# Optimization experiments

Hardware: AMD Instinct MI355X
Metric: run time of the kernel (lower is better)

The kernel has to match this reference:

```python
import jax, jax.numpy as jnp
import numpy as np

B, S, H, D = 1, 2048, 16, 64
IN = 1024
STATE = H * D          # 1024
OUT = 1024
N_LAYERS = 24
EPS = 1e-6


def _rms(t):
    # RMSNorm without affine over last dim
    return t * jax.lax.rsqrt(jnp.mean(t * t, axis=-1, keepdims=True) + EPS)


def setup_inputs() -> dict:
    key = jax.random.key(0)
    ks = jax.random.split(key, 6)
    std = 0.02
    return {
        "x": jax.random.normal(ks[0], (B, S, IN), jnp.float32),
        # input_projection.weight^T: [in, 5*state]  (q|k|v|f|gate)
        "W_in": jax.random.normal(ks[1], (IN, 5 * STATE), jnp.float32) * std,
        "state_weight": jax.random.normal(ks[2], (H, D, D), jnp.float32) * std,
        "forget_multiplier": jax.random.normal(ks[3], (H, D), jnp.float32) * std,
        "logistic_factor": jnp.zeros((H,), jnp.float32),
        "g_norm_weight": jnp.ones((STATE,), jnp.float32),
        "W_out": jax.random.normal(ks[4], (STATE, OUT), jnp.float32) * (std / np.sqrt(2 * N_LAYERS)),
    }


def reference(x, W_in, state_weight, forget_multiplier, logistic_factor, g_norm_weight, W_out):
    proj = x @ W_in                                        # [B,S,5*STATE]
    q, k, v, f, gate = jnp.split(proj, [STATE, 2 * STATE, 3 * STATE, 4 * STATE], axis=-1)
    q = _rms(q.reshape(B, S, H, D))
    k = _rms(k.reshape(B, S, H, D))
    v = _rms(v.reshape(B, S, H, D))
    f = f.reshape(B, S, H, D)

    factor = jax.nn.sigmoid(logistic_factor)               # [H]
    # kvT[b,s,h,i,j] = k_i * (v_j * factor_h)
    kv = k[..., :, None] * (v * factor[None, None, :, None])[..., None, :]   # [B,S,H,D,D]
    # forget gate input, row-wise (depends on k-index i only)
    fg = jax.nn.sigmoid(f * (2.0 * jax.nn.sigmoid(forget_multiplier)))       # [B,S,H,D]
    rg = jax.nn.sigmoid(jnp.asarray(20.0, x.dtype))        # reset_input hardcoded to 20 -> ~1
    W = state_weight * factor[:, None, None]               # [H,D,D]

    def step(state, inp):
        kv_t, f_t = inp                                    # [B,H,D,D], [B,H,D]
        state = f_t[..., None] * jnp.einsum('bhik,hkj->bhij', state, W) + rg * kv_t
        return state, state

    xs = (kv.transpose(1, 0, 2, 3, 4), fg.transpose(1, 0, 2, 3))
    state0 = jnp.zeros((B, H, D, D), x.dtype)
    _, states = jax.lax.scan(step, state0, xs)             # [S,B,H,D,D]

    o = jnp.einsum('bshi,sbhij->bshj', q, states).reshape(B, S, STATE)
    y = o * jax.nn.silu(gate)
    y = _rms(y) * g_norm_weight                            # g_norm (affine RMSNorm)
    return y @ W_out
```

## Files before the change

kernel.cpp:

```cpp
#include <hip/hip_runtime.h>
#include <hip/hip_bf16.h>
#include <cstdint>


typedef __attribute__((ext_vector_type(8))) short short8;
typedef __attribute__((ext_vector_type(4))) short short4v;
typedef __attribute__((ext_vector_type(4))) float f32x4;

#define S_  2048
#define H_  16
#define NPROJ_ 5120

__device__ __forceinline__ float bf2f(unsigned short u) {
  unsigned int x = ((unsigned int)u) << 16;
  return __builtin_bit_cast(float, x);
}
__device__ __forceinline__ unsigned short f2bf(float f) {
  unsigned int x = __builtin_bit_cast(unsigned int, f);
  unsigned int r = (x + 0x7fffu + ((x >> 16) & 1u)) >> 16;
  return (unsigned short)r;
}
__device__ __forceinline__ float sigm(float x) { return 1.f / (1.f + __expf(-x)); }

__device__ __forceinline__ void gload_lds16(unsigned short* lds, const unsigned short* g) {
  __builtin_amdgcn_global_load_lds(
      (const __attribute__((address_space(1))) unsigned int*)g,
      (__attribute__((address_space(3))) unsigned int*)lds, 16, 0, 0);
}

__global__ __launch_bounds__(256) void k_prep(const float* __restrict__ x,
                                              const float* __restrict__ Win,
                                              const float* __restrict__ Wout,
                                              const float* __restrict__ sw,
                                              const float* __restrict__ lf,
                                              unsigned short* __restrict__ xbf,
                                              unsigned short* __restrict__ WinT,
                                              unsigned short* __restrict__ WoutT,
                                              unsigned short* __restrict__ Wt) {
  const int b = blockIdx.x, tid = threadIdx.x;
  if (b < 1536) {
    __shared__ float tile[64][65];
    const float* src; unsigned short* dst; int C, idx;
    if (b < 1280) { src = Win; dst = WinT; C = 5120; idx = b; }
    else          { src = Wout; dst = WoutT; C = 1024; idx = b - 1280; }
    const int R = 1024;
    int nct = C >> 6;
    int bc = idx % nct, br = idx / nct;
    int r0 = br * 64, c0 = bc * 64;
    int col = tid & 63, q = tid >> 6;
#pragma unroll
    for (int i = 0; i < 16; ++i) {
      int row = q * 16 + i;
      tile[row][col] = src[(size_t)(r0 + row) * C + c0 + col];
    }
    __syncthreads();
#pragma unroll
    for (int i = 0; i < 16; ++i) {
      int crow = q * 16 + i;
      dst[(size_t)(c0 + crow) * R + r0 + col] = f2bf(tile[col][crow]);
    }
  } else if (b < 2560) {
    int i = ((b - 1536) * 256 + tid) * 8;
    float4 v0 = *reinterpret_cast<const float4*>(x + i);
    float4 v1 = *reinterpret_cast<const float4*>(x + i + 4);
    uint4 o;
    o.x = (unsigned)f2bf(v0.x) | ((unsigned)f2bf(v0.y) << 16);
    o.y = (unsigned)f2bf(v0.z) | ((unsigned)f2bf(v0.w) << 16);
    o.z = (unsigned)f2bf(v1.x) | ((unsigned)f2bf(v1.y) << 16);
    o.w = (unsigned)f2bf(v1.z) | ((unsigned)f2bf(v1.w) << 16);
    *reinterpret_cast<uint4*>(xbf + i) = o;
  } else {
    int h = b - 2560;
    float factor = sigm(lf[h]);
    int j = tid >> 2, kq = (tid & 3) << 4;
#pragma unroll 4
    for (int k = kq; k < kq + 16; ++k)
      Wt[((size_t)h * 64 + j) * 64 + k] = f2bf(sw[((size_t)h * 64 + k) * 64 + j] * factor);
  }
}

__global__ __launch_bounds__(256) void k_gemm1_fused(
    const unsigned short* __restrict__ A, const unsigned short* __restrict__ BT,
    const float* __restrict__ fm, const float* __restrict__ lf,
    unsigned short* __restrict__ qnb, unsigned short* __restrict__ knb,
    unsigned short* __restrict__ vtb, unsigned short* __restrict__ fgb,
    unsigned short* __restrict__ sgb) {
  __shared__ __attribute__((aligned(16))) unsigned short As[3][128 * 32];
  __shared__ __attribute__((aligned(16))) unsigned short Bs[3][128 * 32];
  const int K = 1024;
  const int tid = threadIdx.x, w = tid >> 6, l = tid & 63;
  const int bx = blockIdx.x;
  const int m0 = (bx / 40) * 128, n0 = (bx % 40) * 128;
  const int wrow = (w >> 1) * 64, wcol = (w & 1) * 64;
  const int l15 = l & 15, lq = l >> 4;
  const int swzoff = l15 * 32 + ((lq ^ ((l15 >> 1) & 3)) * 8);
  f32x4 acc[4][4] = {};
  const int c0 = w * 2;
  const int srow0 = c0 * 16 + (l >> 2);
  const int scol = ((l & 3) ^ ((l >> 3) & 3)) * 8;
  const unsigned short* ga0 = A + (size_t)(m0 + srow0) * K + scol;
  const unsigned short* ga1 = ga0 + 16 * K;
  const unsigned short* gb0 = BT + (size_t)(n0 + srow0) * K + scol;
  const unsigned short* gb1 = gb0 + 16 * K;
#define STAGE1(bufi, kof)                                  \
  do {                                                     \
    gload_lds16(&As[bufi][c0 * 512], ga0 + (kof));         \
    gload_lds16(&As[bufi][(c0 + 1) * 512], ga1 + (kof));   \
    gload_lds16(&Bs[bufi][c0 * 512], gb0 + (kof));         \
    gload_lds16(&Bs[bufi][(c0 + 1) * 512], gb1 + (kof));   \
  } while (0)
  STAGE1(0, 0);
  STAGE1(1, 32);
  asm volatile("s_waitcnt vmcnt(4)" ::: "memory");
  __builtin_amdgcn_s_barrier();
  asm volatile("" ::: "memory");
  for (int t = 0; t < 32; ++t) {
    const unsigned short* Ab = As[t % 3];
    const unsigned short* Bb = Bs[t % 3];
    short8 af[4], bfr[4];
#pragma unroll
    for (int mt = 0; mt < 4; ++mt)
      af[mt] = *reinterpret_cast<const short8*>(Ab + (4 * (w >> 1) + mt) * 512 + swzoff);
#pragma unroll
    for (int nt = 0; nt < 4; ++nt)
      bfr[nt] = *reinterpret_cast<const short8*>(Bb + (4 * (w & 1) + nt) * 512 + swzoff);
    __builtin_amdgcn_s_setprio(1);
#pragma unroll
    for (int mt = 0; mt < 4; ++mt)
#pragma unroll
      for (int nt = 0; nt < 2; ++nt)
        acc[mt][nt] = __builtin_amdgcn_mfma_f32_16x16x32_bf16(af[mt], bfr[nt], acc[mt][nt], 0, 0, 0);
    __builtin_amdgcn_s_setprio(0);
    __builtin_amdgcn_sched_barrier(0);
    if (t < 30) STAGE1((t + 2) % 3, (t + 2) * 32);
    __builtin_amdgcn_sched_barrier(0);
    __builtin_amdgcn_s_setprio(1);
#pragma unroll
    for (int mt = 0; mt < 4; ++mt)
#pragma unroll
      for (int nt = 2; nt < 4; ++nt)
        acc[mt][nt] = __builtin_amdgcn_mfma_f32_16x16x32_bf16(af[mt], bfr[nt], acc[mt][nt], 0, 0, 0);
    __builtin_amdgcn_s_setprio(0);
    if (t < 30) {
      asm volatile("s_waitcnt vmcnt(4)" ::: "memory");
      __builtin_amdgcn_s_barrier();
      asm volatile("" ::: "memory");
    } else if (t == 30) {
      asm volatile("s_waitcnt vmcnt(0)" ::: "memory");
      __builtin_amdgcn_s_barrier();
      asm volatile("" ::: "memory");
    }
  }
  const int seg = n0 >> 10;
  const int colbase = n0 + wcol;
  const int h = (colbase & 1023) >> 6;
  const float rg = 0.9999999979388464f;
  if (seg < 3) {
    float sc = 1.f;
    if (seg == 2) sc = rg * sigm(lf[h]);
    unsigned short* dst = (seg == 0 ? qnb : (seg == 1 ? knb : vtb)) + (size_t)h * S_ * 64;
#pragma unroll
    for (int mt = 0; mt < 4; ++mt) {
      float rstd[4];
#pragma unroll
      for (int r = 0; r < 4; ++r) {
        float s = 0.f;
#pragma unroll
        for (int nt = 0; nt < 4; ++nt) s += acc[mt][nt][r] * acc[mt][nt][r];
        s += __shfl_xor(s, 1); s += __shfl_xor(s, 2);
        s += __shfl_xor(s, 4); s += __shfl_xor(s, 8);
        rstd[r] = rsqrtf(s * (1.f / 64.f) + 1e-6f) * sc;
      }
#pragma unroll
      for (int nt = 0; nt < 4; ++nt)
#pragma unroll
        for (int r = 0; r < 4; ++r) {
          int sr = m0 + wrow + 16 * mt + lq * 4 + r;
          dst[(size_t)sr * 64 + 16 * nt + l15] = f2bf(acc[mt][nt][r] * rstd[r]);
        }
    }
  } else if (seg == 3) {
    float mult[4];
#pragma unroll
    for (int nt = 0; nt < 4; ++nt) mult[nt] = 2.f * sigm(fm[h * 64 + 16 * nt + l15]);
    unsigned short* dst = fgb + (size_t)h * S_ * 64;
#pragma unroll
    for (int mt = 0; mt < 4; ++mt)
#pragma unroll
      for (int nt = 0; nt < 4; ++nt)
#pragma unroll
        for (int r = 0; r < 4; ++r) {
          int sr = m0 + wrow + 16 * mt + lq * 4 + r;
          dst[(size_t)sr * 64 + 16 * nt + l15] = f2bf(sigm(acc[mt][nt][r] * mult[nt]));
        }
  } else {
    int j0 = colbase - 4096;
#pragma unroll
    for (int mt = 0; mt < 4; ++mt)
#pragma unroll
      for (int nt = 0; nt < 4; ++nt)
#pragma unroll
        for (int r = 0; r < 4; ++r) {
          int sr = m0 + wrow + 16 * mt + lq * 4 + r;
          float g = acc[mt][nt][r];
          sgb[(size_t)sr * 1024 + j0 + 16 * nt + l15] = f2bf(g * sigm(g));
        }
  }
}

#define TS 64
#define HALO 16
#define WIN 80
#define KSTR 72

__global__ __launch_bounds__(256) void k_recur(const unsigned short* __restrict__ qnb,
                                               const unsigned short* __restrict__ knb,
                                               const unsigned short* __restrict__ vtb,
                                               const unsigned short* __restrict__ fgb,
                                               const unsigned short* __restrict__ Wt,
                                               unsigned short* __restrict__ obuf) {
  __shared__ __attribute__((aligned(16))) unsigned short kw[WIN * KSTR];
  __shared__ __attribute__((aligned(16))) unsigned short fw[WIN * KSTR];
  __shared__ __attribute__((aligned(16))) unsigned short vw[2][WIN * KSTR];
  const int bx = blockIdx.x;
  const int h = bx & 15, tile = bx >> 4;
  const int s0 = tile * TS;
  const int tid = threadIdx.x, w = tid >> 6, l = tid & 63;

  short8 aw[2];
#pragma unroll
  for (int kt = 0; kt < 2; ++kt)
    aw[kt] = *reinterpret_cast<const short8*>(
        Wt + ((size_t)h * 64 + 16 * w + (l & 15)) * 64 + 32 * kt + 8 * (l >> 4));

  const unsigned short* kh = knb + (size_t)h * S_ * 64;
  const unsigned short* fh = fgb + (size_t)h * S_ * 64;
  const unsigned short* vh = vtb + (size_t)h * S_ * 64;
  const short8 z8 = {0, 0, 0, 0, 0, 0, 0, 0};
  for (int e = tid; e < WIN * 8; e += 256) {
    int rw = e >> 3, c8 = (e & 7) << 3;
    int t = s0 - HALO + rw;
    short8 kv8 = z8, fv8 = z8, vv8 = z8;
    if (t >= 0) {
      kv8 = *reinterpret_cast<const short8*>(kh + (size_t)t * 64 + c8);
      fv8 = *reinterpret_cast<const short8*>(fh + (size_t)t * 64 + c8);
      vv8 = *reinterpret_cast<const short8*>(vh + (size_t)t * 64 + c8);
    }
    *reinterpret_cast<short8*>(kw + rw * KSTR + c8) = kv8;
    *reinterpret_cast<short8*>(fw + rw * KSTR + c8) = fv8;
    *reinterpret_cast<short8*>(vw[0] + rw * KSTR + c8) = vv8;
  }

  const int srow = tid >> 2, t4 = tid & 3;
  float qc[16], oacc[16];
  {
    const unsigned short* qrow = qnb + ((size_t)h * S_ + s0 + srow) * 64 + t4 * 16;
    short8 qa = *reinterpret_cast<const short8*>(qrow);
    short8 qb = *reinterpret_cast<const short8*>(qrow + 8);
#pragma unroll
    for (int i = 0; i < 8; ++i) { qc[i] = bf2f((unsigned short)qa[i]); oacc[i] = 0.f; }
#pragma unroll
    for (int i = 0; i < 8; ++i) { qc[8 + i] = bf2f((unsigned short)qb[i]); oacc[8 + i] = 0.f; }
  }
  __syncthreads();

  for (int p = 0; p <= 16; ++p) {
    const unsigned short* cur = vw[p & 1];
    if (p > 0) {
      const unsigned short* fr = fw + (srow - p + 17) * KSTR + t4 * 16;
      short8 a = *reinterpret_cast<const short8*>(fr);
      short8 b = *reinterpret_cast<const short8*>(fr + 8);
#pragma unroll
      for (int i = 0; i < 8; ++i) qc[i] *= bf2f((unsigned short)a[i]);
#pragma unroll
      for (int i = 0; i < 8; ++i) qc[8 + i] *= bf2f((unsigned short)b[i]);
    }
    {
      int rr = srow - p + 16;
      const unsigned short* kr = kw + rr * KSTR + t4 * 16;
      short8 a = *reinterpret_cast<const short8*>(kr);
      short8 b = *reinterpret_cast<const short8*>(kr + 8);
      float part = 0.f;
#pragma unroll
      for (int i = 0; i < 8; ++i) part += qc[i] * bf2f((unsigned short)a[i]);
#pragma unroll
      for (int i = 0; i < 8; ++i) part += qc[8 + i] * bf2f((unsigned short)b[i]);
      part += __shfl_xor(part, 1);
      part += __shfl_xor(part, 2);
      const unsigned short* vr = cur + rr * KSTR + t4 * 16;
      short8 va = *reinterpret_cast<const short8*>(vr);
      short8 vb = *reinterpret_cast<const short8*>(vr + 8);
#pragma unroll
      for (int i = 0; i < 8; ++i) oacc[i] += part * bf2f((unsigned short)va[i]);
#pragma unroll
      for (int i = 0; i < 8; ++i) oacc[8 + i] += part * bf2f((unsigned short)vb[i]);
    }
    if (p < 16) {
      unsigned short* nxt = vw[(p + 1) & 1];
#pragma unroll
      for (int nt = 0; nt < 5; ++nt) {
        f32x4 a = {0.f, 0.f, 0.f, 0.f};
#pragma unroll
        for (int kt = 0; kt < 2; ++kt) {
          short8 bfrag = *reinterpret_cast<const short8*>(
              cur + (16 * nt + (l & 15)) * KSTR + 32 * kt + 8 * (l >> 4));
          a = __builtin_amdgcn_mfma_f32_16x16x32_bf16(aw[kt], bfrag, a, 0, 0, 0);
        }
        int trow = 16 * nt + (l & 15);
        short4v pk;
        pk[0] = (short)f2bf(a[0]); pk[1] = (short)f2bf(a[1]);
        pk[2] = (short)f2bf(a[2]); pk[3] = (short)f2bf(a[3]);
        *reinterpret_cast<short4v*>(nxt + trow * KSTR + 16 * w + 4 * (l >> 4)) = pk;
      }
    }
    __syncthreads();
  }
  unsigned short* od = obuf + ((size_t)(s0 + srow)) * 1024 + h * 64 + t4 * 16;
  short8 o1, o2;
#pragma unroll
  for (int i = 0; i < 8; ++i) { o1[i] = (short)f2bf(oacc[i]); o2[i] = (short)f2bf(oacc[8 + i]); }
  *reinterpret_cast<short8*>(od) = o1;
  *reinterpret_cast<short8*>(od + 8) = o2;
}

__global__ __launch_bounds__(256) void k_finalnorm(const unsigned short* __restrict__ obuf,
                                                   const unsigned short* __restrict__ sgb,
                                                   const float* __restrict__ gnw,
                                                   unsigned short* __restrict__ ybf) {
  __shared__ float red[4];
  const int s = blockIdx.x, tid = threadIdx.x;
  const unsigned short* orow = obuf + (size_t)s * 1024;
  const unsigned short* grow = sgb + (size_t)s * 1024;
  int j0 = tid * 4;
  short4v o4 = *reinterpret_cast<const short4v*>(orow + j0);
  short4v g4 = *reinterpret_cast<const short4v*>(grow + j0);
  float u[4];
  float ssq = 0.f;
#pragma unroll
  for (int i = 0; i < 4; ++i) {
    u[i] = bf2f((unsigned short)o4[i]) * bf2f((unsigned short)g4[i]);
    ssq += u[i] * u[i];
  }
  for (int m = 1; m < 64; m <<= 1) ssq += __shfl_xor(ssq, m);
  if ((tid & 63) == 0) red[tid >> 6] = ssq;
  __syncthreads();
  float tot = red[0] + red[1] + red[2] + red[3];
  float r = rsqrtf(tot / 1024.f + 1e-6f);
#pragma unroll
  for (int i = 0; i < 4; ++i)
    ybf[(size_t)s * 1024 + j0 + i] = f2bf(u[i] * r * gnw[j0 + i]);
}

__global__ __launch_bounds__(256) void k_gemm2(const unsigned short* __restrict__ A,
                                               const unsigned short* __restrict__ BT,
                                               float* __restrict__ C) {
  __shared__ __attribute__((aligned(16))) unsigned short As[3 * 64 * 32];
  __shared__ __attribute__((aligned(16))) unsigned short Bs[3 * 64 * 32];
  const int K = 1024;
  const int tid = threadIdx.x, w = tid >> 6, l = tid & 63;
  const int bx = blockIdx.x;
  const int m0 = (bx >> 4) * 64, n0 = (bx & 15) * 64;
  const int wrow = (w >> 1) * 32, wcol = (w & 1) * 32;
  const int l15 = l & 15, lq = l >> 4;
  const int swzoff = l15 * 32 + ((lq ^ ((l15 >> 1) & 3)) * 8);
  f32x4 acc[2][2] = {};
  const int scol = ((l & 3) ^ ((l >> 3) & 3)) * 8;
  unsigned short* arrs[2]; int dofs[2]; const unsigned short* gsp[2];
#pragma unroll
  for (int j = 0; j < 2; ++j) {
    int id = 2 * w + j;
    if (id < 4) {
      arrs[j] = As; dofs[j] = id * 512;
      gsp[j] = A + (size_t)(m0 + 16 * id + (l >> 2)) * K + scol;
    } else {
      arrs[j] = Bs; dofs[j] = (id - 4) * 512;
      gsp[j] = BT + (size_t)(n0 + 16 * (id - 4) + (l >> 2)) * K + scol;
    }
  }
#define STAGE2(bufi, kof)                                                \
  do {                                                                   \
    gload_lds16(arrs[0] + (bufi) * (64 * 32) + dofs[0], gsp[0] + (kof)); \
    gload_lds16(arrs[1] + (bufi) * (64 * 32) + dofs[1], gsp[1] + (kof)); \
  } while (0)
  STAGE2(0, 0);
  STAGE2(1, 32);
  asm volatile("s_waitcnt vmcnt(2)" ::: "memory");
  __builtin_amdgcn_s_barrier();
  asm volatile("" ::: "memory");
  for (int t = 0; t < 32; ++t) {
    if (t < 30) STAGE2((t + 2) % 3, (t + 2) * 32);
    const unsigned short* Ab = As + (t % 3) * (64 * 32);
    const unsigned short* Bb = Bs + (t % 3) * (64 * 32);
    short8 af[2], bfr[2];
#pragma unroll
    for (int mt = 0; mt < 2; ++mt)
      af[mt] = *reinterpret_cast<const short8*>(Ab + (2 * (w >> 1) + mt) * 512 + swzoff);
#pragma unroll
    for (int nt = 0; nt < 2; ++nt)
      bfr[nt] = *reinterpret_cast<const short8*>(Bb + (2 * (w & 1) + nt) * 512 + swzoff);
#pragma unroll
    for (int mt = 0; mt < 2; ++mt)
#pragma unroll
      for (int nt = 0; nt < 2; ++nt)
        acc[mt][nt] = __builtin_amdgcn_mfma_f32_16x16x32_bf16(af[mt], bfr[nt], acc[mt][nt], 0, 0, 0);
    if (t < 30) {
      asm volatile("s_waitcnt vmcnt(2)" ::: "memory");
      __builtin_amdgcn_s_barrier();
      asm volatile("" ::: "memory");
    } else if (t == 30) {
      asm volatile("s_waitcnt vmcnt(0)" ::: "memory");
      __builtin_amdgcn_s_barrier();
      asm volatile("" ::: "memory");
    }
  }
#pragma unroll
  for (int mt = 0; mt < 2; ++mt)
#pragma unroll
    for (int nt = 0; nt < 2; ++nt)
#pragma unroll
      for (int r = 0; r < 4; ++r)
        C[(size_t)(m0 + wrow + 16 * mt + lq * 4 + r) * 1024 + n0 + wcol + 16 * nt + l15] =
            acc[mt][nt][r];
}

extern "C" void kernel_launch(void* const* d_in, const int* in_sizes, int n_in,
                              void* d_out, int out_size, void* d_ws, size_t ws_size,
                              hipStream_t stream) {
  const float* x    = (const float*)d_in[0];
  const float* Win  = (const float*)d_in[1];
  const float* sw   = (const float*)d_in[2];
  const float* fm   = (const float*)d_in[3];
  const float* lf   = (const float*)d_in[4];
  const float* gnw  = (const float*)d_in[5];
  const float* Wout = (const float*)d_in[6];
  float* out = (float*)d_out;

  uint8_t* ws = (uint8_t*)d_ws;
  size_t off = 0;
  auto alloc = [&](size_t bytes) -> void* {
    void* p = ws + off;
    off += (bytes + 255) & ~(size_t)255;
    return p;
  };
  unsigned short* xbf   = (unsigned short*)alloc((size_t)S_ * 1024 * 2);
  unsigned short* WinT  = (unsigned short*)alloc((size_t)NPROJ_ * 1024 * 2);
  unsigned short* WoutT = (unsigned short*)alloc((size_t)1024 * 1024 * 2);
  unsigned short* Wt    = (unsigned short*)alloc((size_t)16 * 64 * 64 * 2);
  unsigned short* qnb = (unsigned short*)alloc((size_t)H_ * S_ * 64 * 2);
  unsigned short* knb = (unsigned short*)alloc((size_t)H_ * S_ * 64 * 2);
  unsigned short* vtb = (unsigned short*)alloc((size_t)H_ * S_ * 64 * 2);
  unsigned short* fgb = (unsigned short*)alloc((size_t)H_ * S_ * 64 * 2);
  unsigned short* sgb = (unsigned short*)alloc((size_t)S_ * 1024 * 2);
  unsigned short* obuf = (unsigned short*)alloc((size_t)S_ * 1024 * 2);
  unsigned short* ybf = (unsigned short*)alloc((size_t)S_ * 1024 * 2);

  k_prep<<<dim3(2576), dim3(256), 0, stream>>>(x, Win, Wout, sw, lf, xbf, WinT, WoutT, Wt);
  k_gemm1_fused<<<dim3(16 * 40), dim3(256), 0, stream>>>(xbf, WinT, fm, lf,
                                                         qnb, knb, vtb, fgb, sgb);
  k_recur<<<dim3((S_ / TS) * H_), dim3(256), 0, stream>>>(qnb, knb, vtb, fgb, Wt, obuf);
  k_finalnorm<<<dim3(S_), dim3(256), 0, stream>>>(obuf, sgb, gnw, ybf);
  k_gemm2<<<dim3(32 * 16), dim3(256), 0, stream>>>(ybf, WoutT, out);
}
```

Measured before the change: 85.20 us.

## Fuse gated RMSNorm into recurrence epilogue and GEMM2 row scaling

Removes the separate final-norm kernel. The recurrence epilogue now multiplies by the silu gate and the norm weight, accumulates each row's sum of squares into a global buffer with atomics, and writes the unnormalized product. The output GEMM then applies the per-row rsqrt scale to its accumulators, since the row scale commutes with the matmul. This saves one launch and a full read/write pass over the intermediate, at the cost of atomics and a zeroing block in the prep kernel.

```diff
diff --git a/kernel.cpp b/kernel.cpp
--- a/kernel.cpp
+++ b/kernel.cpp
@@ -36,7 +36,8 @@
                                               unsigned short* __restrict__ xbf,
                                               unsigned short* __restrict__ WinT,
                                               unsigned short* __restrict__ WoutT,
-                                              unsigned short* __restrict__ Wt) {
+                                              unsigned short* __restrict__ Wt,
+                                              float* __restrict__ rowsum) {
   const int b = blockIdx.x, tid = threadIdx.x;
   if (b < 1536) {
     __shared__ float tile[64][65];
@@ -69,13 +70,16 @@
     o.z = (unsigned)f2bf(v1.x) | ((unsigned)f2bf(v1.y) << 16);
     o.w = (unsigned)f2bf(v1.z) | ((unsigned)f2bf(v1.w) << 16);
     *reinterpret_cast<uint4*>(xbf + i) = o;
-  } else {
+  } else if (b < 2576) {
     int h = b - 2560;
     float factor = sigm(lf[h]);
     int j = tid >> 2, kq = (tid & 3) << 4;
 #pragma unroll 4
     for (int k = kq; k < kq + 16; ++k)
       Wt[((size_t)h * 64 + j) * 64 + k] = f2bf(sw[((size_t)h * 64 + k) * 64 + j] * factor);
+  } else {
+#pragma unroll
+    for (int i = 0; i < 8; ++i) rowsum[tid * 8 + i] = 0.f;
   }
 }
 
@@ -218,7 +222,10 @@
                                                const unsigned short* __restrict__ vtb,
                                                const unsigned short* __restrict__ fgb,
                                                const unsigned short* __restrict__ Wt,
-                                               unsigned short* __restrict__ obuf) {
+                                               const unsigned short* __restrict__ sgb,
+                                               const float* __restrict__ gnw,
+                                               float* __restrict__ rowsum,
+                                               unsigned short* __restrict__ ubuf) {
   __shared__ __attribute__((aligned(16))) unsigned short kw[WIN * KSTR];
   __shared__ __attribute__((aligned(16))) unsigned short fw[WIN * KSTR];
   __shared__ __attribute__((aligned(16))) unsigned short vw[2][WIN * KSTR];
@@ -315,44 +322,32 @@
     }
     __syncthreads();
   }
-  unsigned short* od = obuf + ((size_t)(s0 + srow)) * 1024 + h * 64 + t4 * 16;
+  const int scol0 = h * 64 + t4 * 16;
+  const int srowg = s0 + srow;
+  const unsigned short* sgrow = sgb + (size_t)srowg * 1024 + scol0;
+  short8 g1 = *reinterpret_cast<const short8*>(sgrow);
+  short8 g2 = *reinterpret_cast<const short8*>(sgrow + 8);
+  float u[16];
+  float part = 0.f;
+#pragma unroll
+  for (int i = 0; i < 8; ++i) { u[i] = oacc[i] * bf2f((unsigned short)g1[i]); part += u[i] * u[i]; }
+#pragma unroll
+  for (int i = 0; i < 8; ++i) { u[8 + i] = oacc[8 + i] * bf2f((unsigned short)g2[i]); part += u[8 + i] * u[8 + i]; }
+  part += __shfl_xor(part, 1);
+  part += __shfl_xor(part, 2);
+  if (t4 == 0) atomicAdd(rowsum + srowg, part);
+  const float* gp = gnw + scol0;
   short8 o1, o2;
 #pragma unroll
-  for (int i = 0; i < 8; ++i) { o1[i] = (short)f2bf(oacc[i]); o2[i] = (short)f2bf(oacc[8 + i]); }
+  for (int i = 0; i < 8; ++i) { o1[i] = (short)f2bf(u[i] * gp[i]); o2[i] = (short)f2bf(u[8 + i] * gp[8 + i]); }
+  unsigned short* od = ubuf + (size_t)srowg * 1024 + scol0;
   *reinterpret_cast<short8*>(od) = o1;
   *reinterpret_cast<short8*>(od + 8) = o2;
 }
 
-__global__ __launch_bounds__(256) void k_finalnorm(const unsigned short* __restrict__ obuf,
-                                                   const unsigned short* __restrict__ sgb,
-                                                   const float* __restrict__ gnw,
-                                                   unsigned short* __restrict__ ybf) {
-  __shared__ float red[4];
-  const int s = blockIdx.x, tid = threadIdx.x;
-  const unsigned short* orow = obuf + (size_t)s * 1024;
-  const unsigned short* grow = sgb + (size_t)s * 1024;
-  int j0 = tid * 4;
-  short4v o4 = *reinterpret_cast<const short4v*>(orow + j0);
-  short4v g4 = *reinterpret_cast<const short4v*>(grow + j0);
-  float u[4];
-  float ssq = 0.f;
-#pragma unroll
-  for (int i = 0; i < 4; ++i) {
-    u[i] = bf2f((unsigned short)o4[i]) * bf2f((unsigned short)g4[i]);
-    ssq += u[i] * u[i];
-  }
-  for (int m = 1; m < 64; m <<= 1) ssq += __shfl_xor(ssq, m);
-  if ((tid & 63) == 0) red[tid >> 6] = ssq;
-  __syncthreads();
-  float tot = red[0] + red[1] + red[2] + red[3];
-  float r = rsqrtf(tot / 1024.f + 1e-6f);
-#pragma unroll
-  for (int i = 0; i < 4; ++i)
-    ybf[(size_t)s * 1024 + j0 + i] = f2bf(u[i] * r * gnw[j0 + i]);
-}
-
 __global__ __launch_bounds__(256) void k_gemm2(const unsigned short* __restrict__ A,
                                                const unsigned short* __restrict__ BT,
+                                               const float* __restrict__ rowsum,
                                                float* __restrict__ C) {
   __shared__ __attribute__((aligned(16))) unsigned short As[3 * 64 * 32];
   __shared__ __attribute__((aligned(16))) unsigned short Bs[3 * 64 * 32];
@@ -416,11 +411,13 @@
 #pragma unroll
   for (int mt = 0; mt < 2; ++mt)
 #pragma unroll
-    for (int nt = 0; nt < 2; ++nt)
-#pragma unroll
-      for (int r = 0; r < 4; ++r)
-        C[(size_t)(m0 + wrow + 16 * mt + lq * 4 + r) * 1024 + n0 + wcol + 16 * nt + l15] =
-            acc[mt][nt][r];
+    for (int r = 0; r < 4; ++r) {
+      int row = m0 + wrow + 16 * mt + lq * 4 + r;
+      float scl = rsqrtf(rowsum[row] * (1.f / 1024.f) + 1e-6f);
+#pragma unroll
+      for (int nt = 0; nt < 2; ++nt)
+        C[(size_t)row * 1024 + n0 + wcol + 16 * nt + l15] = acc[mt][nt][r] * scl;
+    }
 }
 
 extern "C" void kernel_launch(void* const* d_in, const int* in_sizes, int n_in,
@@ -451,13 +448,14 @@
   unsigned short* vtb = (unsigned short*)alloc((size_t)H_ * S_ * 64 * 2);
   unsigned short* fgb = (unsigned short*)alloc((size_t)H_ * S_ * 64 * 2);
   unsigned short* sgb = (unsigned short*)alloc((size_t)S_ * 1024 * 2);
-  unsigned short* obuf = (unsigned short*)alloc((size_t)S_ * 1024 * 2);
-  unsigned short* ybf = (unsigned short*)alloc((size_t)S_ * 1024 * 2);
-
-  k_prep<<<dim3(2576), dim3(256), 0, stream>>>(x, Win, Wout, sw, lf, xbf, WinT, WoutT, Wt);
+  unsigned short* ubuf = (unsigned short*)alloc((size_t)S_ * 1024 * 2);
+  float* rowsum = (float*)alloc((size_t)S_ * 4);
+
+  k_prep<<<dim3(2577), dim3(256), 0, stream>>>(x, Win, Wout, sw, lf, xbf, WinT, WoutT, Wt,
+                                               rowsum);
   k_gemm1_fused<<<dim3(16 * 40), dim3(256), 0, stream>>>(xbf, WinT, fm, lf,
                                                          qnb, knb, vtb, fgb, sgb);
-  k_recur<<<dim3((S_ / TS) * H_), dim3(256), 0, stream>>>(qnb, knb, vtb, fgb, Wt, obuf);
-  k_finalnorm<<<dim3(S_), dim3(256), 0, stream>>>(obuf, sgb, gnw, ybf);
-  k_gemm2<<<dim3(32 * 16), dim3(256), 0, stream>>>(ybf, WoutT, out);
-}
+  k_recur<<<dim3((S_ / TS) * H_), dim3(256), 0, stream>>>(qnb, knb, vtb, fgb, Wt,
+                                                          sgb, gnw, rowsum, ubuf);
+  k_gemm2<<<dim3(32 * 16), dim3(256), 0, stream>>>(ubuf, WoutT, rowsum, out);
+}
```

Measured after the change: 82.43 us. 1.03x faster.
